# Kernel optimization log

Measured on AMD Instinct MI355X. Metric: run time of the kernel, lower is better.

Reference implementation:

```python
import jax, jax.numpy as jnp
import numpy as np

EMBED_DIM = 1024
NUM_HEADS = 16
HEAD_DIM = EMBED_DIM // NUM_HEADS


def setup_inputs() -> dict:
    key = jax.random.key(0)
    ks = jax.random.split(key, 9)
    B, P, E = 4, 1024, EMBED_DIM
    s = 1.0 / np.sqrt(E)
    return {
        "x": jax.random.normal(ks[0], (B, P, E), dtype=jnp.float32),
        "Wq": jax.random.normal(ks[1], (E, E), dtype=jnp.float32) * s,
        "bq": jnp.zeros((E,), dtype=jnp.float32),
        "Wk": jax.random.normal(ks[2], (E, E), dtype=jnp.float32) * s,
        "bk": jnp.zeros((E,), dtype=jnp.float32),
        "Wv": jax.random.normal(ks[3], (E, E), dtype=jnp.float32) * s,
        "bv": jnp.zeros((E,), dtype=jnp.float32),
        "Wo": jax.random.normal(ks[4], (E, E), dtype=jnp.float32) * s,
        "bo": jnp.zeros((E,), dtype=jnp.float32),
    }


def reference(x, Wq, bq, Wk, bk, Wv, bv, Wo, bo):
    B, P, E = x.shape
    A, D = NUM_HEADS, HEAD_DIM
    scale = jnp.asarray(np.sqrt(D), dtype=x.dtype)
    # torch Linear: y = x @ W.T + b
    q = (x @ Wq.T + bq).reshape(B, P, A, D).transpose(0, 2, 1, 3)  # (B,A,P,D)
    k = (x @ Wk.T + bk).reshape(B, P, A, D).transpose(0, 2, 1, 3)
    v = (x @ Wv.T + bv).reshape(B, P, A, D).transpose(0, 2, 1, 3)
    scores = jnp.einsum("bapd,baqd->bapq", q, k) / scale  # (B,A,P,P)
    attn = jax.nn.softmax(scores, axis=-1)
    out = jnp.einsum("bapq,baqd->bapd", attn, v)  # (B,A,P,D)
    out = out.transpose(0, 2, 1, 3).reshape(B, P, E)
    return out @ Wo.T + bo
```

## Files before the change

### kernel.cpp

```cpp
#include <hip/hip_runtime.h>
#include <stdint.h>

typedef unsigned short u16;
typedef short short4v __attribute__((ext_vector_type(4)));
typedef short short8v __attribute__((ext_vector_type(8)));
typedef float float4v __attribute__((ext_vector_type(4)));

#define AS1(p) ((__attribute__((address_space(1))) void*)(p))
#define AS3(p) ((__attribute__((address_space(3))) void*)(p))

#define MFMA32(a, b, c) __builtin_amdgcn_mfma_f32_16x16x32_bf16(a, b, c, 0, 0, 0)

static __device__ __forceinline__ float4v MFMA16(short4v a, short4v b, float4v c) {
#if __has_builtin(__builtin_amdgcn_mfma_f32_16x16x16bf16_1k)
  return __builtin_amdgcn_mfma_f32_16x16x16bf16_1k(a, b, c, 0, 0, 0);
#else
  float4v d;
  asm volatile("v_mfma_f32_16x16x16_bf16 %0, %1, %2, %3\n\ts_nop 7\n\ts_nop 3"
               : "=v"(d)
               : "v"(a), "v"(b), "v"(c));
  return d;
#endif
}

static __device__ __forceinline__ u16 f2bf(float f) {
  uint32_t u = __builtin_bit_cast(uint32_t, f);
  u += 0x7FFFu + ((u >> 16) & 1u);
  return (u16)(u >> 16);
}

static __device__ __forceinline__ unsigned cvtpk(float lo, float hi) {
  unsigned r;
  asm("v_cvt_pk_bf16_f32 %0, %1, %2" : "=v"(r) : "v"(lo), "v"(hi));
  return r;
}

#define TR4(v0_, v1_, v2_, v3_, addr_)                                   \
  asm volatile("ds_read_b64_tr_b16 %0, %4 offset:0\n\t"                  \
               "ds_read_b64_tr_b16 %1, %4 offset:2048\n\t"               \
               "ds_read_b64_tr_b16 %2, %4 offset:4096\n\t"               \
               "ds_read_b64_tr_b16 %3, %4 offset:6144\n\t"               \
               "s_waitcnt lgkmcnt(0)"                                    \
               : "=&v"(v0_), "=&v"(v1_), "=&v"(v2_), "=&v"(v3_)          \
               : "v"(addr_)                                              \
               : "memory")


__global__ __launch_bounds__(256) void cast1_k(const float* __restrict__ s, u16* __restrict__ d) {
  const int i = (blockIdx.x * 256 + threadIdx.x) * 4;
  float4v v = *(const float4v*)(s + i);
  short4v o;
#pragma unroll
  for (int j = 0; j < 4; j++) o[j] = (short)f2bf(v[j]);
  *(short4v*)(d + i) = o;
}

__global__ __launch_bounds__(256) void cast4_k(const float* __restrict__ s0, const float* __restrict__ s1,
                                               const float* __restrict__ s2, const float* __restrict__ s3,
                                               u16* __restrict__ d0, u16* __restrict__ d1,
                                               u16* __restrict__ d2, u16* __restrict__ d3) {
  const float* s;
  u16* d;
  switch (blockIdx.y) {
    case 0: s = s0; d = d0; break;
    case 1: s = s1; d = d1; break;
    case 2: s = s2; d = d2; break;
    default: s = s3; d = d3; break;
  }
  const int i = (blockIdx.x * 256 + threadIdx.x) * 4;
  float4v v = *(const float4v*)(s + i);
  short4v o;
#pragma unroll
  for (int j = 0; j < 4; j++) o[j] = (short)f2bf(v[j]);
  *(short4v*)(d + i) = o;
}


__global__ __launch_bounds__(512, 2) void gemm256(
    const u16* __restrict__ A,
    const u16* __restrict__ B0, const u16* __restrict__ B1, const u16* __restrict__ B2,
    const float* __restrict__ bias0, const float* __restrict__ bias1, const float* __restrict__ bias2,
    u16* __restrict__ C0, u16* __restrict__ C1, u16* __restrict__ C2,
    float sc0, float sc1, float sc2) {
  constexpr int K = 1024;
  __shared__ u16 As[4][256][32];
  __shared__ u16 Bs[4][256][32];

  const int t = threadIdx.x;
  const int lane = t & 63, wid = t >> 6;
  const int wm = wid >> 2, wn = wid & 3;
  const int lr = lane & 15, g = lane >> 4;

  const int id = blockIdx.x;
  const int xc = id & 7, off = id >> 3;
  const int mb = (xc & 3) * 4 + (off & 3);
  const int nbt = (xc >> 2) * 6 + (off >> 2);
  const int seg = nbt >> 2, nb = nbt & 3;

  const u16* Bm = seg == 0 ? B0 : (seg == 1 ? B1 : B2);
  const float* bias = seg == 0 ? bias0 : (seg == 1 ? bias1 : bias2);
  u16* C = seg == 0 ? C0 : (seg == 1 ? C1 : C2);
  const float scale = seg == 0 ? sc0 : (seg == 1 ? sc1 : sc2);

  const u16* Ap = A + (size_t)mb * 256 * K;
  const u16* Bp = Bm + (size_t)nb * 256 * K;

  float4v z = {0.f, 0.f, 0.f, 0.f};
  float4v acc[8][4];
#pragma unroll
  for (int i = 0; i < 8; i++)
#pragma unroll
    for (int j = 0; j < 4; j++) acc[i][j] = z;

  const int ar0 = t >> 2, ar1 = ar0 + 128, ac0 = (t & 3) * 8;

#define STGA(rg, kb)                                                                                              \
  {                                                                                                               \
    __builtin_amdgcn_global_load_lds(AS1(Ap + (size_t)ar0 * K + (kb) + ac0), AS3(&As[rg][ar0][ac0]), 16, 0, 0);   \
    __builtin_amdgcn_global_load_lds(AS1(Ap + (size_t)ar1 * K + (kb) + ac0), AS3(&As[rg][ar1][ac0]), 16, 0, 0);   \
  }
#define STGB(rg, kb)                                                                                              \
  {                                                                                                               \
    __builtin_amdgcn_global_load_lds(AS1(Bp + (size_t)ar0 * K + (kb) + ac0), AS3(&Bs[rg][ar0][ac0]), 16, 0, 0);   \
    __builtin_amdgcn_global_load_lds(AS1(Bp + (size_t)ar1 * K + (kb) + ac0), AS3(&Bs[rg][ar1][ac0]), 16, 0, 0);   \
  }
#define VM4 asm volatile("s_waitcnt vmcnt(4)" ::: "memory")
#define VM0 asm volatile("s_waitcnt vmcnt(0)" ::: "memory")

#define PH(rg, mq, STG_, VM_)                                                         \
  {                                                                                   \
    short8v a_[4], b_[4];                                                             \
    _Pragma("unroll") for (int i = 0; i < 4; i++)                                     \
        a_[i] = *(const short8v*)&As[rg][wm * 128 + ((mq)*4 + i) * 16 + lr][g * 8];   \
    _Pragma("unroll") for (int j = 0; j < 4; j++)                                     \
        b_[j] = *(const short8v*)&Bs[rg][wn * 64 + j * 16 + lr][g * 8];               \
    STG_;                                                                             \
    VM_;                                                                              \
    __builtin_amdgcn_s_barrier();                                                     \
    asm volatile("s_waitcnt lgkmcnt(0)");                                             \
    __builtin_amdgcn_sched_barrier(0);                                                \
    __builtin_amdgcn_s_setprio(1);                                                    \
    _Pragma("unroll") for (int i = 0; i < 4; i++)                                     \
        _Pragma("unroll") for (int j = 0; j < 4; j++)                                 \
            acc[(mq)*4 + i][j] = MFMA32(a_[i], b_[j], acc[(mq)*4 + i][j]);            \
    __builtin_amdgcn_s_setprio(0);                                                    \
    __builtin_amdgcn_s_barrier();                                                     \
    __builtin_amdgcn_sched_barrier(0);                                                \
  }

  STGA(0, 0);
  STGB(0, 0);
  STGA(1, 32);
  STGB(1, 32);
  VM4;
  __builtin_amdgcn_s_barrier();

  for (int it = 0; it < 15; ++it) {
    const int r0 = (it & 1) << 1, r1 = r0 + 1;
    const int rn2 = ((it + 1) & 1) << 1, rn3 = rn2 + 1;
    const int kb2 = it * 64 + 64, kb3 = kb2 + 32;
    PH(r0, 0, STGA(rn2, kb2), );
    PH(r0, 1, STGB(rn2, kb2), VM4);
    PH(r1, 0, STGA(rn3, kb3), );
    PH(r1, 1, STGB(rn3, kb3), VM4);
  }
  PH(2, 0, , );
  PH(2, 1, , VM0);
  PH(3, 0, , );
  PH(3, 1, , );

#undef PH
#undef STGA
#undef STGB

  const int colb = nb * 256 + wn * 64;
  const int rowb = mb * 256 + wm * 128;
#pragma unroll
  for (int j = 0; j < 4; j++) {
    const int col = colb + j * 16 + lr;
    const float bv = bias[col];
#pragma unroll
    for (int i = 0; i < 8; i++) {
      const int row0 = rowb + i * 16 + g * 4;
#pragma unroll
      for (int r = 0; r < 4; r++)
        C[(size_t)(row0 + r) * 1024 + col] = f2bf((acc[i][j][r] + bv) * scale);
    }
  }
}


template <int OUTF32>
__global__ __launch_bounds__(256) void gemm_bt(
    const u16* __restrict__ A,
    const u16* __restrict__ B0, const u16* __restrict__ B1, const u16* __restrict__ B2,
    const float* __restrict__ bias0, const float* __restrict__ bias1, const float* __restrict__ bias2,
    void* __restrict__ C0, void* __restrict__ C1, void* __restrict__ C2,
    float sc0, float sc1, float sc2) {
  constexpr int K = 1024;
  __shared__ u16 As[2][128 * 32];
  __shared__ u16 Bs[2][128 * 32];

  const int t = threadIdx.x;
  const int lane = t & 63, wid = t >> 6;
  const int wr = wid >> 1, wc = wid & 1;
  const int lr = lane & 15, g = lane >> 4;

  const int seg = blockIdx.y >> 3, nb = blockIdx.y & 7, mb = blockIdx.x;
  const u16* B = seg == 0 ? B0 : (seg == 1 ? B1 : B2);
  const float* bias = seg == 0 ? bias0 : (seg == 1 ? bias1 : bias2);
  void* C = seg == 0 ? C0 : (seg == 1 ? C1 : C2);
  const float scale = seg == 0 ? sc0 : (seg == 1 ? sc1 : sc2);

  const u16* Ap = A + (size_t)mb * 128 * K;
  const u16* Bp = B + (size_t)nb * 128 * K;

  float4v z = {0.f, 0.f, 0.f, 0.f};
  float4v acc[4][4];
#pragma unroll
  for (int i = 0; i < 4; i++)
#pragma unroll
    for (int j = 0; j < 4; j++) acc[i][j] = z;

  const int r0 = t >> 2, c0 = (t & 3) * 8;

#define GSTAGE(u, kk)                                                                                          \
  do {                                                                                                         \
    __builtin_amdgcn_global_load_lds(AS1(Ap + (size_t)r0 * K + (kk) + c0), AS3(&As[u][t * 8]), 16, 0, 0);      \
    __builtin_amdgcn_global_load_lds(AS1(Ap + (size_t)(r0 + 64) * K + (kk) + c0), AS3(&As[u][(t + 256) * 8]),  \
                                     16, 0, 0);                                                                \
    __builtin_amdgcn_global_load_lds(AS1(Bp + (size_t)r0 * K + (kk) + c0), AS3(&Bs[u][t * 8]), 16, 0, 0);      \
    __builtin_amdgcn_global_load_lds(AS1(Bp + (size_t)(r0 + 64) * K + (kk) + c0), AS3(&Bs[u][(t + 256) * 8]),  \
                                     16, 0, 0);                                                                \
  } while (0)

  GSTAGE(0, 0);
  int cur = 0;
  for (int k0 = 0; k0 < K; k0 += 32) {
    __syncthreads();
    if (k0 + 32 < K) GSTAGE(cur ^ 1, k0 + 32);

    const u16* Au = &As[cur][0];
    const u16* Bu = &Bs[cur][0];
    short8v af[4], bfr[4];
#pragma unroll
    for (int mi = 0; mi < 4; mi++) af[mi] = *(const short8v*)(Au + (wr * 64 + mi * 16 + lr) * 32 + g * 8);
#pragma unroll
    for (int ni = 0; ni < 4; ni++) bfr[ni] = *(const short8v*)(Bu + (wc * 64 + ni * 16 + lr) * 32 + g * 8);
    __builtin_amdgcn_s_setprio(1);
#pragma unroll
    for (int mi = 0; mi < 4; mi++)
#pragma unroll
      for (int ni = 0; ni < 4; ni++) acc[mi][ni] = MFMA32(af[mi], bfr[ni], acc[mi][ni]);
    __builtin_amdgcn_s_setprio(0);
    __syncthreads();
    cur ^= 1;
  }
#undef GSTAGE

  const int colb = nb * 128 + wc * 64;
  const int rowb = mb * 128 + wr * 64;
#pragma unroll
  for (int ni = 0; ni < 4; ni++) {
    const int col = colb + ni * 16 + lr;
    const float bv = bias[col];
#pragma unroll
    for (int mi = 0; mi < 4; mi++) {
      const int row0 = rowb + mi * 16 + g * 4;
      float4v a = acc[mi][ni];
      if (OUTF32) {
        float* Cf = (float*)C;
#pragma unroll
        for (int r = 0; r < 4; r++) Cf[(size_t)(row0 + r) * 1024 + col] = (a[r] + bv) * scale;
      } else {
        u16* Cb = (u16*)C;
#pragma unroll
        for (int r = 0; r < 4; r++) Cb[(size_t)(row0 + r) * 1024 + col] = f2bf((a[r] + bv) * scale);
      }
    }
  }
}


__global__ __launch_bounds__(256) void attn_fwd(const u16* __restrict__ Qm, const u16* __restrict__ Km,
                                                const u16* __restrict__ Vm, u16* __restrict__ Om) {
  __shared__ u16 Ks[2][64 * 64];
  __shared__ u16 Vs[2][64 * 64];

  const int t = threadIdx.x;
  const int lane = t & 63, w = t >> 6;
  const int lr = lane & 15, g = lane >> 4;
  const int qb = blockIdx.x, pair = blockIdx.y;
  const int b = pair >> 4, a = pair & 15;

  const int qrow = qb * 64 + w * 16 + lr;
  const size_t qoff = ((size_t)(b * 1024 + qrow)) * 1024 + a * 64;
  const short8v qf0 = *(const short8v*)(Qm + qoff + g * 8);
  const short8v qf1 = *(const short8v*)(Qm + qoff + 32 + g * 8);

  float4v z = {0.f, 0.f, 0.f, 0.f};
  float4v ot[4];
#pragma unroll
  for (int i = 0; i < 4; i++) ot[i] = z;
  float mrun = -3.0e38f, lsum = 0.f;

  const u16* Kb = Km + ((size_t)b * 1024) * 1024 + a * 64;
  const u16* Vb = Vm + ((size_t)b * 1024) * 1024 + a * 64;

  const int kr0 = t >> 3, kr1 = kr0 + 32;
  const int kc0 = ((t & 7) ^ (kr0 & 7)) * 8;
  const int vr0 = (t >> 1) & 63;
  const int vc0 = (t >> 7) * 16 + (t & 1) * 8;

#define ASTAGE(u, kt)                                                                                             \
  do {                                                                                                            \
    __builtin_amdgcn_global_load_lds(AS1(Kb + (size_t)((kt) + kr0) * 1024 + kc0), AS3(&Ks[u][t * 8]), 16, 0, 0);  \
    __builtin_amdgcn_global_load_lds(AS1(Kb + (size_t)((kt) + kr1) * 1024 + kc0), AS3(&Ks[u][(t + 256) * 8]),     \
                                     16, 0, 0);                                                                   \
    __builtin_amdgcn_global_load_lds(AS1(Vb + (size_t)((kt) + vr0) * 1024 + vc0), AS3(&Vs[u][t * 8]), 16, 0, 0);  \
    __builtin_amdgcn_global_load_lds(AS1(Vb + (size_t)((kt) + vr0) * 1024 + vc0 + 32), AS3(&Vs[u][(t + 256) * 8]),\
                                     16, 0, 0);                                                                   \
  } while (0)

  const unsigned vsbase = (unsigned)(uintptr_t)AS3(&Vs[0][0]);
  const unsigned vlane = (unsigned)((g * 4 + (lr >> 2)) * 32 + (lane & 3) * 8);

  ASTAGE(0, 0);
  int cur = 0;
  for (int kt = 0; kt < 1024; kt += 64) {
    __syncthreads();
    if (kt + 64 < 1024) ASTAGE(cur ^ 1, kt + 64);

    const u16* Ku = &Ks[cur][0];
    float4v st[4];
#pragma unroll
    for (int jt = 0; jt < 4; jt++) {
      float4v s = z;
      const int row = jt * 16 + lr;
      const int rsw = (row & 7) << 4;
      __builtin_amdgcn_s_setprio(1);
#pragma unroll
      for (int ks = 0; ks < 2; ks++) {
        const int baddr = (row * 128 + (ks * 4 + g) * 16) ^ rsw;
        short8v kf = *(const short8v*)((const char*)Ku + baddr);
        s = MFMA32(kf, ks ? qf1 : qf0, s);
      }
      __builtin_amdgcn_s_setprio(0);
      st[jt] = s;
    }

    float tm = st[0][0];
#pragma unroll
    for (int jt = 0; jt < 4; jt++)
#pragma unroll
      for (int r = 0; r < 4; r++) tm = fmaxf(tm, st[jt][r]);
    tm = fmaxf(tm, __shfl_xor(tm, 16));
    tm = fmaxf(tm, __shfl_xor(tm, 32));
    if (!__all(tm - mrun <= 8.f)) {
      const float mnew = fmaxf(mrun, tm);
      const float sca = exp2f(mrun - mnew);
      lsum *= sca;
#pragma unroll
      for (int d = 0; d < 4; d++)
#pragma unroll
        for (int r = 0; r < 4; r++) ot[d][r] *= sca;
      mrun = mnew;
    }
    float p[16];
    float ts = 0.f;
#pragma unroll
    for (int jt = 0; jt < 4; jt++)
#pragma unroll
      for (int r = 0; r < 4; r++) {
        const float pv = exp2f(st[jt][r] - mrun);
        p[jt * 4 + r] = pv;
        ts += pv;
      }
    ts += __shfl_xor(ts, 16);
    ts += __shfl_xor(ts, 32);
    lsum += ts;

    short4v pf[4];
#pragma unroll
    for (int jt = 0; jt < 4; jt++) {
      unsigned lo = cvtpk(p[jt * 4 + 0], p[jt * 4 + 1]);
      unsigned hi = cvtpk(p[jt * 4 + 2], p[jt * 4 + 3]);
      unsigned u2[2] = {lo, hi};
      pf[jt] = __builtin_bit_cast(short4v, *(unsigned long long*)u2);
    }

    unsigned va = vsbase + (unsigned)cur * 8192u + vlane;
#pragma unroll
    for (int jt = 0; jt < 4; jt++) {
      short4v vf0, vf1, vf2, vf3;
      TR4(vf0, vf1, vf2, vf3, va);
      __builtin_amdgcn_s_setprio(1);
      ot[0] = MFMA16(vf0, pf[jt], ot[0]);
      ot[1] = MFMA16(vf1, pf[jt], ot[1]);
      ot[2] = MFMA16(vf2, pf[jt], ot[2]);
      ot[3] = MFMA16(vf3, pf[jt], ot[3]);
      __builtin_amdgcn_s_setprio(0);
      va += 512u;
    }

    __syncthreads();
    cur ^= 1;
  }
#undef ASTAGE

  const float inv = 1.f / lsum;
  u16* Op = Om + ((size_t)(b * 1024 + qrow)) * 1024 + a * 64;
#pragma unroll
  for (int dblk = 0; dblk < 4; dblk++) {
    short4v o4;
#pragma unroll
    for (int r = 0; r < 4; r++) o4[r] = (short)f2bf(ot[dblk][r] * inv);
    *(short4v*)(Op + dblk * 16 + g * 4) = o4;
  }
}


extern "C" void kernel_launch(void* const* d_in, const int* in_sizes, int n_in,
                              void* d_out, int out_size, void* d_ws, size_t ws_size,
                              hipStream_t stream) {
  (void)in_sizes; (void)n_in; (void)out_size; (void)ws_size;
  const float* x = (const float*)d_in[0];
  const float* Wq = (const float*)d_in[1];
  const float* bq = (const float*)d_in[2];
  const float* Wk = (const float*)d_in[3];
  const float* bk = (const float*)d_in[4];
  const float* Wv = (const float*)d_in[5];
  const float* bv = (const float*)d_in[6];
  const float* Wo = (const float*)d_in[7];
  const float* bo = (const float*)d_in[8];
  float* out = (float*)d_out;

  char* ws = (char*)d_ws;
  const size_t MB = 1u << 20;
  u16* xb = (u16*)(ws + 0 * MB);
  u16* Wqb = (u16*)(ws + 8 * MB);
  u16* Wkb = (u16*)(ws + 10 * MB);
  u16* Wvb = (u16*)(ws + 12 * MB);
  u16* Wob = (u16*)(ws + 14 * MB);
  u16* Qb = (u16*)(ws + 16 * MB);
  u16* Kb = (u16*)(ws + 24 * MB);
  u16* Vb = (u16*)(ws + 32 * MB);
  u16* Ab = (u16*)(ws + 40 * MB);

  const float csc = 1.4426950408889634f / 8.0f;

  cast1_k<<<4096, 256, 0, stream>>>(x, xb);
  cast4_k<<<dim3(1024, 4), 256, 0, stream>>>(Wq, Wk, Wv, Wo, Wqb, Wkb, Wvb, Wob);
  gemm256<<<192, 512, 0, stream>>>(xb, Wqb, Wkb, Wvb, bq, bk, bv, Qb, Kb, Vb, csc, 1.f, 1.f);
  attn_fwd<<<dim3(16, 64), 256, 0, stream>>>(Qb, Kb, Vb, Ab);
  gemm_bt<1><<<dim3(32, 8), 256, 0, stream>>>(Ab, Wob, Wob, Wob, bo, bo, bo, out, out, out, 1.f, 1.f, 1.f);
}
```

Measured before the change: 201.5 us.

## Swizzle LDS tiles and deepen GEMM prefetch pipeline to three stages

The GEMM now fetches each global 16-byte chunk from an XOR-swizzled column and the fragment reads apply the matching XOR, so LDS reads of the A/B tiles should hit fewer bank conflicts. The main loop is restructured into a 4-buffer ring with three k-slices in flight (vmcnt(8) instead of 4), giving more latency hiding for global-to-LDS loads. A trailing sched_barrier is also removed. This raises outstanding memory traffic and makes the wait-count logic harder to keep correct.

```diff
diff --git a/kernel.cpp b/kernel.cpp
--- a/kernel.cpp
+++ b/kernel.cpp
@@ -112,28 +112,35 @@
 #pragma unroll
     for (int j = 0; j < 4; j++) acc[i][j] = z;
 
-  const int ar0 = t >> 2, ar1 = ar0 + 128, ac0 = (t & 3) * 8;
-
-#define STGA(rg, kb)                                                                                              \
-  {                                                                                                               \
-    __builtin_amdgcn_global_load_lds(AS1(Ap + (size_t)ar0 * K + (kb) + ac0), AS3(&As[rg][ar0][ac0]), 16, 0, 0);   \
-    __builtin_amdgcn_global_load_lds(AS1(Ap + (size_t)ar1 * K + (kb) + ac0), AS3(&As[rg][ar1][ac0]), 16, 0, 0);   \
-  }
-#define STGB(rg, kb)                                                                                              \
-  {                                                                                                               \
-    __builtin_amdgcn_global_load_lds(AS1(Bp + (size_t)ar0 * K + (kb) + ac0), AS3(&Bs[rg][ar0][ac0]), 16, 0, 0);   \
-    __builtin_amdgcn_global_load_lds(AS1(Bp + (size_t)ar1 * K + (kb) + ac0), AS3(&Bs[rg][ar1][ac0]), 16, 0, 0);   \
-  }
+  const int sr0 = t >> 2, sr1 = sr0 + 128;
+  const int pc = (t & 3) * 8;
+  const int scol = ((t & 3) ^ ((t >> 3) & 3)) * 8;
+
+#define STGA(rg, kb)                                                                                            \
+  {                                                                                                             \
+    __builtin_amdgcn_global_load_lds(AS1(Ap + (size_t)sr0 * K + (kb) + scol), AS3(&As[rg][sr0][pc]), 16, 0, 0); \
+    __builtin_amdgcn_global_load_lds(AS1(Ap + (size_t)sr1 * K + (kb) + scol), AS3(&As[rg][sr1][pc]), 16, 0, 0); \
+  }
+#define STGB(rg, kb)                                                                                            \
+  {                                                                                                             \
+    __builtin_amdgcn_global_load_lds(AS1(Bp + (size_t)sr0 * K + (kb) + scol), AS3(&Bs[rg][sr0][pc]), 16, 0, 0); \
+    __builtin_amdgcn_global_load_lds(AS1(Bp + (size_t)sr1 * K + (kb) + scol), AS3(&Bs[rg][sr1][pc]), 16, 0, 0); \
+  }
+#define VM8 asm volatile("s_waitcnt vmcnt(8)" ::: "memory")
 #define VM4 asm volatile("s_waitcnt vmcnt(4)" ::: "memory")
 #define VM0 asm volatile("s_waitcnt vmcnt(0)" ::: "memory")
 
 #define PH(rg, mq, STG_, VM_)                                                         \
   {                                                                                   \
     short8v a_[4], b_[4];                                                             \
-    _Pragma("unroll") for (int i = 0; i < 4; i++)                                     \
-        a_[i] = *(const short8v*)&As[rg][wm * 128 + ((mq)*4 + i) * 16 + lr][g * 8];   \
-    _Pragma("unroll") for (int j = 0; j < 4; j++)                                     \
-        b_[j] = *(const short8v*)&Bs[rg][wn * 64 + j * 16 + lr][g * 8];               \
+    _Pragma("unroll") for (int i = 0; i < 4; i++) {                                   \
+      const int r_ = wm * 128 + ((mq)*4 + i) * 16 + lr;                               \
+      a_[i] = *(const short8v*)&As[rg][r_][(g ^ ((r_ >> 1) & 3)) * 8];                \
+    }                                                                                 \
+    _Pragma("unroll") for (int j = 0; j < 4; j++) {                                   \
+      const int r_ = wn * 64 + j * 16 + lr;                                           \
+      b_[j] = *(const short8v*)&Bs[rg][r_][(g ^ ((r_ >> 1) & 3)) * 8];                \
+    }                                                                                 \
     STG_;                                                                             \
     VM_;                                                                              \
     __builtin_amdgcn_s_barrier();                                                     \
@@ -145,25 +152,24 @@
             acc[(mq)*4 + i][j] = MFMA32(a_[i], b_[j], acc[(mq)*4 + i][j]);            \
     __builtin_amdgcn_s_setprio(0);                                                    \
     __builtin_amdgcn_s_barrier();                                                     \
-    __builtin_amdgcn_sched_barrier(0);                                                \
   }
 
   STGA(0, 0);
   STGB(0, 0);
   STGA(1, 32);
   STGB(1, 32);
-  VM4;
+  STGA(2, 64);
+  STGB(2, 64);
+  VM8;
   __builtin_amdgcn_s_barrier();
 
-  for (int it = 0; it < 15; ++it) {
-    const int r0 = (it & 1) << 1, r1 = r0 + 1;
-    const int rn2 = ((it + 1) & 1) << 1, rn3 = rn2 + 1;
-    const int kb2 = it * 64 + 64, kb3 = kb2 + 32;
-    PH(r0, 0, STGA(rn2, kb2), );
-    PH(r0, 1, STGB(rn2, kb2), VM4);
-    PH(r1, 0, STGA(rn3, kb3), );
-    PH(r1, 1, STGB(rn3, kb3), VM4);
-  }
+  for (int r = 0; r < 29; ++r) {
+    const int rg = r & 3, rs = (r + 3) & 3, kb = (r + 3) * 32;
+    PH(rg, 0, STGA(rs, kb), );
+    PH(rg, 1, STGB(rs, kb), VM8);
+  }
+  PH(1, 0, , );
+  PH(1, 1, , VM4);
   PH(2, 0, , );
   PH(2, 1, , VM0);
   PH(3, 0, , );
```

Measured after the change: 195.4 us. 1.03x faster.
